# Kernel optimization log

Hardware: AMD Instinct MI355X
Metric: run time of the kernel (lower is better)

The kernel has to match this reference:

```python
import jax, jax.numpy as jnp
import numpy as np

B, T, C, S, H, K = 32, 128, 32, 256, 64, 3  # T == 2*H required by final Linear(hidden*2, 1)


def setup_inputs() -> dict:
    key = jax.random.key(0)
    k1, k2, k3, k4 = jax.random.split(key, 4)
    x = jax.random.normal(k1, (B, T, C, S), jnp.float32)
    # ConvLSTMCell: Conv1d(C+H -> 4H, kernel K, padding same), gate order i,f,o,g
    Wc = jax.random.normal(k2, (4 * H, C + H, K), jnp.float32) * 0.05
    bc = jnp.zeros((4 * H,), jnp.float32)
    # final Linear(hidden*2 = T, 1)
    Wl = jax.random.normal(k3, (1, T), jnp.float32) * 0.05
    bl = jnp.zeros((1,), jnp.float32)
    return {"x": x, "Wc": Wc, "bc": bc, "Wl": Wl, "bl": bl}


def _cell(x_t, h, c, Wc, bc):
    # x_t: (B, C, T); h, c: (B, H, T). Conv over the T axis, 'same' padding.
    z = jnp.concatenate([x_t, h], axis=1)  # (B, C+H, T)
    conv = jax.lax.conv_general_dilated(
        z, Wc, window_strides=(1,), padding='SAME',
        dimension_numbers=('NCH', 'OIH', 'NCH')) + bc[None, :, None]
    ci, cf, co, cg = jnp.split(conv, 4, axis=1)
    i = jax.nn.sigmoid(ci)
    f = jax.nn.sigmoid(cf)
    o = jax.nn.sigmoid(co)
    g = jnp.tanh(cg)
    c_next = f * c + i * g
    h_next = o * jnp.tanh(c_next)
    return h_next, c_next


def reference(x, Wc, bc, Wl, bl):
    # x: (B, T, C, S); sequential scan over spatial axis S with (h, c) recurrence.
    xs = jnp.transpose(x, (3, 0, 2, 1))  # (S, B, C, T)
    h0 = jnp.zeros((x.shape[0], H, x.shape[1]), x.dtype)

    def step(carry, xt):
        h, c = carry
        h2, c2 = _cell(xt, h, c, Wc, bc)
        return (h2, c2), h2

    _, hs = jax.lax.scan(step, (h0, h0), xs)  # hs: (S, B, H, T)
    lstm_out = jnp.transpose(hs, (1, 0, 2, 3))  # (B, S, H, T)
    out = jax.nn.sigmoid(jnp.einsum('bsht,ot->bso', lstm_out, Wl)[..., None].squeeze(-1)[..., None] * 0 + jnp.einsum('bsht,ot->bsho', lstm_out, Wl) + bl)
    return out  # (B, S, H, 1)
```

## Files before the change

### kernel.cpp

```cpp
#include <hip/hip_runtime.h>


#define Bb 32
#define Tt 128
#define Cc 32
#define Ss 256
#define Hh 64

typedef __bf16 bf16x8 __attribute__((ext_vector_type(8)));
typedef short  short8 __attribute__((ext_vector_type(8)));
typedef float  f32x4  __attribute__((ext_vector_type(4)));
typedef unsigned short u16;
typedef unsigned int   u32;

__device__ __forceinline__ u16 f2bf(float f) {
    u32 u = __float_as_uint(f);
    u = (u + 0x7FFFu + ((u >> 16) & 1u)) >> 16;
    return (u16)u;
}
__device__ __forceinline__ float fsig(float x) {
    float e = __expf(-x);
    return __builtin_amdgcn_rcpf(1.0f + e);
}
__device__ __forceinline__ float ftanh_(float x) {
    float e = __expf(2.0f * x);
    return 1.0f - 2.0f * __builtin_amdgcn_rcpf(e + 1.0f);
}

__global__ __launch_bounds__(256) void xpose_kernel(const float* __restrict__ x,
                                                    u16* __restrict__ xT) {
    __shared__ u16 tile[64][130];
    const int tc0 = blockIdx.x * 128;
    const int s0  = blockIdx.y * 64;
    const int b   = blockIdx.z;
    const int tid = threadIdx.x;
    const float* xb = x + (size_t)b * (Tt * Cc * Ss);
#pragma unroll
    for (int i = 0; i < 32; ++i) {
        const int tcr = (tid >> 6) + 4 * i;
        const int sr  = tid & 63;
        tile[sr][tcr] = f2bf(xb[(size_t)(tc0 + tcr) * Ss + s0 + sr]);
    }
    __syncthreads();
    u32* xTo = (u32*)(xT + (size_t)b * (Ss * Tt * Cc));
#pragma unroll
    for (int j = 0; j < 16; ++j) {
        const int sw = (tid >> 6) + 4 * j;
        const int tw = (tid & 63) * 2;
        xTo[(((size_t)(s0 + sw)) * (Tt * Cc) + tc0 + tw) >> 1] = *(const u32*)&tile[sw][tw];
    }
}

__global__ __launch_bounds__(512, 2) void convlstm_kernel(
    const float* __restrict__ Wc, const float* __restrict__ bc,
    const float* __restrict__ Wl, const float* __restrict__ bl,
    const u16* __restrict__ xT, float* __restrict__ out) {

    __shared__ u16  zbuf[2][130][104];
    __shared__ float red[8][16];
    __shared__ float bcl[256];

    const int b    = blockIdx.x;
    const int tid  = threadIdx.x;
    const int w    = tid >> 6;
    const int lane = tid & 63;
    const int l15  = lane & 15;
    const int q    = lane >> 4;
    const int ht   = w >> 1;
    const int th   = w & 1;

    {
        u32* z32 = (u32*)&zbuf[0][0][0];
        for (int i = tid; i < (2 * 130 * 104) / 2; i += 512) z32[i] = 0;
    }
    if (tid < 256) bcl[tid] = bc[tid];

    bf16x8 afr[4][3][3];
#pragma unroll
    for (int g = 0; g < 4; ++g) {
#pragma unroll
        for (int k = 0; k < 3; ++k) {
#pragma unroll
            for (int ks = 0; ks < 3; ++ks) {
                const int gc = 64 * g + 16 * ht + l15;
                short8 t;
#pragma unroll
                for (int j = 0; j < 8; ++j) {
                    const int c = 32 * ks + 8 * q + j;
                    t[j] = (short)f2bf(Wc[gc * 288 + c * 3 + k]);
                }
                afr[g][k][ks] = __builtin_bit_cast(bf16x8, t);
            }
        }
    }

    float wlv[4];
#pragma unroll
    for (int nj = 0; nj < 4; ++nj) wlv[nj] = Wl[64 * th + 16 * nj + l15];
    const float bl0 = bl[0];

    float cst[16];
#pragma unroll
    for (int i = 0; i < 16; ++i) cst[i] = 0.0f;

    const int xt = tid >> 2;
    const int xc = (tid & 3) * 8;
    const u16* xTb = xT + (size_t)b * (Ss * Tt * Cc);

    {
        uint4 xv0 = *(const uint4*)(xTb + 0 + xt * 32 + xc);
        __syncthreads();
        *(uint4*)&zbuf[0][1 + xt][xc] = xv0;
        __syncthreads();
    }

    float* outb = out + (size_t)b * (Ss * Hh);
    int p = 0;

    for (int s = 0; s < Ss; ++s) {
        uint4 xv;
        const bool havex = (s + 1) < Ss;
        if (havex) xv = *(const uint4*)(xTb + (size_t)(s + 1) * (Tt * Cc) + xt * 32 + xc);

        if (tid < 64 && s > 0) {
            float v = red[(tid >> 4) * 2][tid & 15] + red[(tid >> 4) * 2 + 1][tid & 15] + bl0;
            outb[(size_t)(s - 1) * Hh + tid] = fsig(v);
        }
        __syncthreads();

        const u16 (*zb)[104] = zbuf[p];
        u16 (*zn)[104] = zbuf[p ^ 1];

        float partial[4] = {0.f, 0.f, 0.f, 0.f};

#pragma unroll
        for (int half = 0; half < 2; ++half) {
            f32x4 acc[4][2];
#pragma unroll
            for (int g = 0; g < 4; ++g)
#pragma unroll
                for (int njl = 0; njl < 2; ++njl)
                    acc[g][njl] = (f32x4){0.f, 0.f, 0.f, 0.f};

#pragma unroll
            for (int njl = 0; njl < 2; ++njl) {
                const int nj = half * 2 + njl;
                const int tb = 64 * th + 16 * nj + l15;
#pragma unroll
                for (int k = 0; k < 3; ++k) {
#pragma unroll
                    for (int ks = 0; ks < 3; ++ks) {
                        bf16x8 bfr = *(const bf16x8*)&zb[tb + k][32 * ks + 8 * q];
                        acc[0][njl] = __builtin_amdgcn_mfma_f32_16x16x32_bf16(afr[0][k][ks], bfr, acc[0][njl], 0, 0, 0);
                        acc[1][njl] = __builtin_amdgcn_mfma_f32_16x16x32_bf16(afr[1][k][ks], bfr, acc[1][njl], 0, 0, 0);
                        acc[2][njl] = __builtin_amdgcn_mfma_f32_16x16x32_bf16(afr[2][k][ks], bfr, acc[2][njl], 0, 0, 0);
                        acc[3][njl] = __builtin_amdgcn_mfma_f32_16x16x32_bf16(afr[3][k][ks], bfr, acc[3][njl], 0, 0, 0);
                    }
                }
            }

#pragma unroll
            for (int njl = 0; njl < 2; ++njl) {
                const int nj = half * 2 + njl;
                u16 hp[4];
#pragma unroll
                for (int r = 0; r < 4; ++r) {
                    const int hl = 4 * q + r;
                    const float ci  = acc[0][njl][r] + bcl[0   + 16 * ht + hl];
                    const float cf  = acc[1][njl][r] + bcl[64  + 16 * ht + hl];
                    const float cop = acc[2][njl][r] + bcl[128 + 16 * ht + hl];
                    const float cg  = acc[3][njl][r] + bcl[192 + 16 * ht + hl];
                    const float ig = fsig(ci);
                    const float fg = fsig(cf);
                    const float og = fsig(cop);
                    const float gg = ftanh_(cg);
                    const float cv = fg * cst[nj * 4 + r] + ig * gg;
                    cst[nj * 4 + r] = cv;
                    const float hv = og * ftanh_(cv);
                    partial[r] += hv * wlv[nj];
                    hp[r] = f2bf(hv);
                }
                uint2 hw;
                hw.x = (u32)hp[0] | ((u32)hp[1] << 16);
                hw.y = (u32)hp[2] | ((u32)hp[3] << 16);
                *(uint2*)&zn[1 + 64 * th + 16 * nj + l15][32 + 16 * ht + 4 * q] = hw;
            }
        }

        if (havex) *(uint4*)&zn[1 + xt][xc] = xv;

#pragma unroll
        for (int r = 0; r < 4; ++r) {
#pragma unroll
            for (int off = 1; off <= 8; off <<= 1)
                partial[r] += __shfl_xor(partial[r], off, 64);
        }
        if (l15 == 0) {
#pragma unroll
            for (int r = 0; r < 4; ++r) red[w][4 * q + r] = partial[r];
        }
        __syncthreads();
        p ^= 1;
    }

    if (tid < 64) {
        float v = red[(tid >> 4) * 2][tid & 15] + red[(tid >> 4) * 2 + 1][tid & 15] + bl0;
        outb[(size_t)(Ss - 1) * Hh + tid] = fsig(v);
    }
}

extern "C" void kernel_launch(void* const* d_in, const int* in_sizes, int n_in,
                              void* d_out, int out_size, void* d_ws, size_t ws_size,
                              hipStream_t stream) {
    const float* x  = (const float*)d_in[0];
    const float* Wc = (const float*)d_in[1];
    const float* bc = (const float*)d_in[2];
    const float* Wl = (const float*)d_in[3];
    const float* bl = (const float*)d_in[4];
    float* out = (float*)d_out;
    u16*   xT  = (u16*)d_ws;

    dim3 tgrid(Tt * Cc / 128, Ss / 64, Bb);
    xpose_kernel<<<tgrid, 256, 0, stream>>>(x, xT);
    convlstm_kernel<<<Bb, 512, 0, stream>>>(Wc, bc, Wl, bl, xT, out);
}
```

Before: 1.273 ms.

## Precompute input-to-gate convolution in parallel kernel, shrink recurrent GEMM to hidden part

Splits the gate convolution into an input part and a recurrent part. The input part does not depend on the recurrence, so a new fully parallel kernel computes it for all timesteps and stores it in bf16 in workspace. The sequential kernel then only multiplies the hidden state (K=64 instead of 96) and loads the precomputed gate contributions one step ahead, software-pipelining the MFMA work against the gate math. The cost is about 512MB of extra global traffic, an extra bf16 rounding of the gate pre-activations, and a dependence on the workspace being large enough, with a fallback to the old kernel otherwise.

```diff
diff --git a/kernel.cpp b/kernel.cpp
--- a/kernel.cpp
+++ b/kernel.cpp
@@ -18,6 +18,8 @@
     u = (u + 0x7FFFu + ((u >> 16) & 1u)) >> 16;
     return (u16)u;
 }
+__device__ __forceinline__ float bfl(u32 d) { return __uint_as_float(d << 16); }
+__device__ __forceinline__ float bfh(u32 d) { return __uint_as_float(d & 0xffff0000u); }
 __device__ __forceinline__ float fsig(float x) {
     float e = __expf(-x);
     return __builtin_amdgcn_rcpf(1.0f + e);
@@ -48,6 +50,224 @@
         const int sw = (tid >> 6) + 4 * j;
         const int tw = (tid & 63) * 2;
         xTo[(((size_t)(s0 + sw)) * (Tt * Cc) + tc0 + tw) >> 1] = *(const u32*)&tile[sw][tw];
+    }
+}
+
+__global__ __launch_bounds__(256) void gatex_kernel(
+    const float* __restrict__ Wc, const float* __restrict__ bc,
+    const u16* __restrict__ xT, u16* __restrict__ gateX) {
+
+    __shared__ u16 zx[130][40];
+    const int s   = blockIdx.x;
+    const int b   = blockIdx.y;
+    const int tid = threadIdx.x;
+    const int g   = tid >> 6;
+    const int lane = tid & 63;
+    const int l15 = lane & 15;
+    const int q   = lane >> 4;
+
+    if (tid < 40) {
+        u32* zp = (u32*)&zx[(tid < 20) ? 0 : 129][0];
+        zp[(tid < 20) ? tid : tid - 20] = 0;
+    }
+    const u16* xp = xT + ((size_t)b * Ss + s) * (Tt * Cc);
+#pragma unroll
+    for (int i = 0; i < 4; ++i) {
+        const int idx = tid + 256 * i;
+        const int e = idx * 4;
+        *(uint2*)&zx[1 + (e >> 5)][e & 31] = *(const uint2*)(xp + e);
+    }
+
+    bf16x8 afr[4][3];
+#pragma unroll
+    for (int mt = 0; mt < 4; ++mt)
+#pragma unroll
+        for (int k = 0; k < 3; ++k) {
+            const int gc = 64 * g + 16 * mt + l15;
+            short8 t;
+#pragma unroll
+            for (int j = 0; j < 8; ++j) t[j] = (short)f2bf(Wc[gc * 288 + (8 * q + j) * 3 + k]);
+            afr[mt][k] = __builtin_bit_cast(bf16x8, t);
+        }
+    f32x4 bcv[4];
+#pragma unroll
+    for (int mt = 0; mt < 4; ++mt) bcv[mt] = *(const f32x4*)&bc[64 * g + 16 * mt + 4 * q];
+
+    __syncthreads();
+
+    u16* gxo = gateX + ((size_t)b * Ss + s) * (64 * 128 * 4);
+#pragma unroll
+    for (int nt = 0; nt < 8; ++nt) {
+        f32x4 acc[4];
+#pragma unroll
+        for (int mt = 0; mt < 4; ++mt) acc[mt] = bcv[mt];
+#pragma unroll
+        for (int k = 0; k < 3; ++k) {
+            bf16x8 bfr = *(const bf16x8*)&zx[16 * nt + l15 + k][8 * q];
+            acc[0] = __builtin_amdgcn_mfma_f32_16x16x32_bf16(afr[0][k], bfr, acc[0], 0, 0, 0);
+            acc[1] = __builtin_amdgcn_mfma_f32_16x16x32_bf16(afr[1][k], bfr, acc[1], 0, 0, 0);
+            acc[2] = __builtin_amdgcn_mfma_f32_16x16x32_bf16(afr[2][k], bfr, acc[2], 0, 0, 0);
+            acc[3] = __builtin_amdgcn_mfma_f32_16x16x32_bf16(afr[3][k], bfr, acc[3], 0, 0, 0);
+        }
+#pragma unroll
+        for (int mt = 0; mt < 4; ++mt) {
+            uint2 hw;
+            hw.x = (u32)f2bf(acc[mt][0]) | ((u32)f2bf(acc[mt][1]) << 16);
+            hw.y = (u32)f2bf(acc[mt][2]) | ((u32)f2bf(acc[mt][3]) << 16);
+            const int gcq = 16 * g + 4 * mt + q;
+            *(uint2*)(gxo + ((size_t)gcq * 128 + 16 * nt + l15) * 4) = hw;
+        }
+    }
+}
+
+__global__ __launch_bounds__(512, 2) void convlstm_gx_kernel(
+    const float* __restrict__ Wc, const float* __restrict__ Wl,
+    const float* __restrict__ bl, const u16* __restrict__ gateX,
+    float* __restrict__ out) {
+
+    __shared__ u16  zbuf[2][130][72];
+    __shared__ float red[2][8][16];
+
+    const int b    = blockIdx.x;
+    const int tid  = threadIdx.x;
+    const int w    = tid >> 6;
+    const int lane = tid & 63;
+    const int l15  = lane & 15;
+    const int q    = lane >> 4;
+    const int ht   = w >> 1;
+    const int th   = w & 1;
+
+    {
+        u32* z32 = (u32*)&zbuf[0][0][0];
+        for (int i = tid; i < (2 * 130 * 72) / 2; i += 512) z32[i] = 0;
+    }
+
+    bf16x8 afr[4][3][2];
+#pragma unroll
+    for (int g = 0; g < 4; ++g)
+#pragma unroll
+        for (int k = 0; k < 3; ++k)
+#pragma unroll
+            for (int ks = 0; ks < 2; ++ks) {
+                const int gc = 64 * g + 16 * ht + l15;
+                short8 t;
+#pragma unroll
+                for (int j = 0; j < 8; ++j)
+                    t[j] = (short)f2bf(Wc[gc * 288 + (32 + 32 * ks + 8 * q + j) * 3 + k]);
+                afr[g][k][ks] = __builtin_bit_cast(bf16x8, t);
+            }
+
+    float wlv[4];
+#pragma unroll
+    for (int nj = 0; nj < 4; ++nj) wlv[nj] = Wl[64 * th + 16 * nj + l15];
+    const float bl0 = bl[0];
+
+    float cst[16];
+#pragma unroll
+    for (int i = 0; i < 16; ++i) cst[i] = 0.0f;
+
+    const u16* gxb = gateX + (size_t)b * Ss * (64 * 128 * 4);
+    int off[16];
+#pragma unroll
+    for (int nj = 0; nj < 4; ++nj)
+#pragma unroll
+        for (int g = 0; g < 4; ++g)
+            off[nj * 4 + g] = (((16 * g + 4 * ht + q) * 128) + 64 * th + 16 * nj + l15) * 4;
+
+    uint2 gx[16];
+#pragma unroll
+    for (int i = 0; i < 16; ++i) gx[i] = *(const uint2*)(gxb + off[i]);
+
+    __syncthreads();
+
+    float* outb = out + (size_t)b * (Ss * Hh);
+
+    for (int s = 0; s < Ss; ++s) {
+        if (tid < 64 && s > 0) {
+            const int ps = (s - 1) & 1;
+            float v = red[ps][(tid >> 4) * 2][tid & 15] + red[ps][(tid >> 4) * 2 + 1][tid & 15] + bl0;
+            outb[(size_t)(s - 1) * Hh + tid] = fsig(v);
+        }
+
+        const u16 (*zb)[72] = zbuf[(s & 1) ^ 1];
+        u16 (*zn)[72] = zbuf[s & 1];
+
+        float partial[4] = {0.f, 0.f, 0.f, 0.f};
+        f32x4 acc[2][4];
+
+#pragma unroll
+        for (int c = 0; c < 5; ++c) {
+            if (c < 4) {
+                {
+                    const uint2 v0 = gx[c * 4 + 0], v1 = gx[c * 4 + 1];
+                    const uint2 v2 = gx[c * 4 + 2], v3 = gx[c * 4 + 3];
+                    acc[c & 1][0] = (f32x4){bfl(v0.x), bfh(v0.x), bfl(v0.y), bfh(v0.y)};
+                    acc[c & 1][1] = (f32x4){bfl(v1.x), bfh(v1.x), bfl(v1.y), bfh(v1.y)};
+                    acc[c & 1][2] = (f32x4){bfl(v2.x), bfh(v2.x), bfl(v2.y), bfh(v2.y)};
+                    acc[c & 1][3] = (f32x4){bfl(v3.x), bfh(v3.x), bfl(v3.y), bfh(v3.y)};
+                }
+                if (c == 3 && s + 1 < Ss) {
+                    const u16* gs = gxb + (size_t)(s + 1) * (64 * 128 * 4);
+#pragma unroll
+                    for (int i = 0; i < 16; ++i) gx[i] = *(const uint2*)(gs + off[i]);
+                }
+                {
+                    const int tb = 64 * th + 16 * c + l15;
+#pragma unroll
+                    for (int k = 0; k < 3; ++k)
+#pragma unroll
+                        for (int ks = 0; ks < 2; ++ks) {
+                            bf16x8 bfr = *(const bf16x8*)&zb[tb + k][32 * ks + 8 * q];
+                            acc[c & 1][0] = __builtin_amdgcn_mfma_f32_16x16x32_bf16(afr[0][k][ks], bfr, acc[c & 1][0], 0, 0, 0);
+                            acc[c & 1][1] = __builtin_amdgcn_mfma_f32_16x16x32_bf16(afr[1][k][ks], bfr, acc[c & 1][1], 0, 0, 0);
+                            acc[c & 1][2] = __builtin_amdgcn_mfma_f32_16x16x32_bf16(afr[2][k][ks], bfr, acc[c & 1][2], 0, 0, 0);
+                            acc[c & 1][3] = __builtin_amdgcn_mfma_f32_16x16x32_bf16(afr[3][k][ks], bfr, acc[c & 1][3], 0, 0, 0);
+                        }
+                }
+            }
+            if (c > 0) {
+                const int nj = c - 1;
+                u16 hp[4];
+#pragma unroll
+                for (int r = 0; r < 4; ++r) {
+                    const float ci  = acc[nj & 1][0][r];
+                    const float cf  = acc[nj & 1][1][r];
+                    const float cop = acc[nj & 1][2][r];
+                    const float cg  = acc[nj & 1][3][r];
+                    const float ig = fsig(ci);
+                    const float fg = fsig(cf);
+                    const float og = fsig(cop);
+                    const float gg = ftanh_(cg);
+                    const float cv = fg * cst[nj * 4 + r] + ig * gg;
+                    cst[nj * 4 + r] = cv;
+                    const float hv = og * ftanh_(cv);
+                    partial[r] += hv * wlv[nj];
+                    hp[r] = f2bf(hv);
+                }
+                uint2 hw;
+                hw.x = (u32)hp[0] | ((u32)hp[1] << 16);
+                hw.y = (u32)hp[2] | ((u32)hp[3] << 16);
+                *(uint2*)&zn[1 + 64 * th + 16 * nj + l15][16 * ht + 4 * q] = hw;
+            }
+        }
+
+#pragma unroll
+        for (int r = 0; r < 4; ++r) {
+#pragma unroll
+            for (int offl = 1; offl <= 8; offl <<= 1)
+                partial[r] += __shfl_xor(partial[r], offl, 64);
+        }
+        if (l15 == 0) {
+#pragma unroll
+            for (int r = 0; r < 4; ++r) red[s & 1][w][4 * q + r] = partial[r];
+        }
+        __syncthreads();
+    }
+
+    if (tid < 64) {
+        const int ps = (Ss - 1) & 1;
+        float v = red[ps][(tid >> 4) * 2][tid & 15] + red[ps][(tid >> 4) * 2 + 1][tid & 15] + bl0;
+        outb[(size_t)(Ss - 1) * Hh + tid] = fsig(v);
     }
 }
 
@@ -192,8 +412,8 @@
 #pragma unroll
         for (int r = 0; r < 4; ++r) {
 #pragma unroll
-            for (int off = 1; off <= 8; off <<= 1)
-                partial[r] += __shfl_xor(partial[r], off, 64);
+            for (int offl = 1; offl <= 8; offl <<= 1)
+                partial[r] += __shfl_xor(partial[r], offl, 64);
         }
         if (l15 == 0) {
 #pragma unroll
@@ -218,9 +438,19 @@
     const float* Wl = (const float*)d_in[3];
     const float* bl = (const float*)d_in[4];
     float* out = (float*)d_out;
-    u16*   xT  = (u16*)d_ws;
+
+    u16* xT = (u16*)d_ws;
+    const size_t XT_BYTES = (size_t)Bb * Ss * Tt * Cc * 2;
+    const size_t GX_BYTES = (size_t)Bb * Ss * 4 * Hh * Tt * 2;
 
     dim3 tgrid(Tt * Cc / 128, Ss / 64, Bb);
     xpose_kernel<<<tgrid, 256, 0, stream>>>(x, xT);
-    convlstm_kernel<<<Bb, 512, 0, stream>>>(Wc, bc, Wl, bl, xT, out);
-}
+
+    if (ws_size >= XT_BYTES + GX_BYTES) {
+        u16* gateX = (u16*)((char*)d_ws + XT_BYTES);
+        gatex_kernel<<<dim3(Ss, Bb), 256, 0, stream>>>(Wc, bc, xT, gateX);
+        convlstm_gx_kernel<<<Bb, 512, 0, stream>>>(Wc, Wl, bl, gateX, out);
+    } else {
+        convlstm_kernel<<<Bb, 512, 0, stream>>>(Wc, bc, Wl, bl, xT, out);
+    }
+}
```

Result: no change. 1.273 ms (+0.0%).

## Software-pipeline MFMA and gate math, drop one barrier per step, fold bias

Applied to the files above, without the earlier changes.

Restructures the per-step loop so the MFMA chunk for the next 16-column tile is issued before the gate math of the previous tile, letting matrix and vector work overlap. It removes one __syncthreads per recurrence step by double-buffering the reduction array. It also preloads the bias into the accumulator instead of reading it from LDS, changes the LDS row stride to 136 (likely to reduce bank conflicts), and packs bf16 with a hardware convert instruction. The costs are higher register pressure from two live accumulator sets and reliance on inline asm.

```diff
diff --git a/kernel.cpp b/kernel.cpp
--- a/kernel.cpp
+++ b/kernel.cpp
@@ -6,6 +6,7 @@
 #define Cc 32
 #define Ss 256
 #define Hh 64
+#define ZST 136
 
 typedef __bf16 bf16x8 __attribute__((ext_vector_type(8)));
 typedef short  short8 __attribute__((ext_vector_type(8)));
@@ -25,6 +26,11 @@
 __device__ __forceinline__ float ftanh_(float x) {
     float e = __expf(2.0f * x);
     return 1.0f - 2.0f * __builtin_amdgcn_rcpf(e + 1.0f);
+}
+__device__ __forceinline__ u32 cvtpk(float lo, float hi) {
+    u32 d;
+    asm("v_cvt_pk_bf16_f32 %0, %1, %2" : "=v"(d) : "v"(lo), "v"(hi));
+    return d;
 }
 
 __global__ __launch_bounds__(256) void xpose_kernel(const float* __restrict__ x,
@@ -51,14 +57,13 @@
     }
 }
 
-__global__ __launch_bounds__(512, 2) void convlstm_kernel(
+__global__ __launch_bounds__(512, 2) void convlstm3_kernel(
     const float* __restrict__ Wc, const float* __restrict__ bc,
     const float* __restrict__ Wl, const float* __restrict__ bl,
     const u16* __restrict__ xT, float* __restrict__ out) {
 
-    __shared__ u16  zbuf[2][130][104];
-    __shared__ float red[8][16];
-    __shared__ float bcl[256];
+    __shared__ u16  zbuf[2][130][ZST];
+    __shared__ float red[2][8][16];
 
     const int b    = blockIdx.x;
     const int tid  = threadIdx.x;
@@ -71,32 +76,38 @@
 
     {
         u32* z32 = (u32*)&zbuf[0][0][0];
-        for (int i = tid; i < (2 * 130 * 104) / 2; i += 512) z32[i] = 0;
-    }
-    if (tid < 256) bcl[tid] = bc[tid];
+        for (int i = tid; i < (2 * 130 * ZST) / 2; i += 512) z32[i] = 0;
+    }
 
     bf16x8 afr[4][3][3];
 #pragma unroll
-    for (int g = 0; g < 4; ++g) {
-#pragma unroll
-        for (int k = 0; k < 3; ++k) {
+    for (int g = 0; g < 4; ++g)
+#pragma unroll
+        for (int k = 0; k < 3; ++k)
 #pragma unroll
             for (int ks = 0; ks < 3; ++ks) {
                 const int gc = 64 * g + 16 * ht + l15;
                 short8 t;
 #pragma unroll
-                for (int j = 0; j < 8; ++j) {
-                    const int c = 32 * ks + 8 * q + j;
-                    t[j] = (short)f2bf(Wc[gc * 288 + c * 3 + k]);
-                }
-                afr[g][k][ks] = __builtin_bit_cast(bf16x8, t);
+                for (int j = 0; j < 8; ++j)
+                    t[j] = (short)f2bf(Wc[gc * 288 + (32 * ks + 8 * q + j) * 3 + k]);
+                f32x4 kv = __builtin_bit_cast(f32x4, t);
+                asm volatile("" : "+v"(kv));
+                afr[g][k][ks] = __builtin_bit_cast(bf16x8, kv);
             }
-        }
-    }
-
+
+    f32x4 bcv[4];
+#pragma unroll
+    for (int g = 0; g < 4; ++g) {
+        bcv[g] = *(const f32x4*)&bc[64 * g + 16 * ht + 4 * q];
+        asm volatile("" : "+v"(bcv[g]));
+    }
     float wlv[4];
 #pragma unroll
-    for (int nj = 0; nj < 4; ++nj) wlv[nj] = Wl[64 * th + 16 * nj + l15];
+    for (int nj = 0; nj < 4; ++nj) {
+        wlv[nj] = Wl[64 * th + 16 * nj + l15];
+        asm volatile("" : "+v"(wlv[nj]));
+    }
     const float bl0 = bl[0];
 
     float cst[16];
@@ -108,14 +119,13 @@
     const u16* xTb = xT + (size_t)b * (Ss * Tt * Cc);
 
     {
-        uint4 xv0 = *(const uint4*)(xTb + 0 + xt * 32 + xc);
+        uint4 xv0 = *(const uint4*)(xTb + xt * 32 + xc);
         __syncthreads();
-        *(uint4*)&zbuf[0][1 + xt][xc] = xv0;
+        *(uint4*)&zbuf[1][1 + xt][xc] = xv0;
         __syncthreads();
     }
 
     float* outb = out + (size_t)b * (Ss * Hh);
-    int p = 0;
 
     for (int s = 0; s < Ss; ++s) {
         uint4 xv;
@@ -123,66 +133,51 @@
         if (havex) xv = *(const uint4*)(xTb + (size_t)(s + 1) * (Tt * Cc) + xt * 32 + xc);
 
         if (tid < 64 && s > 0) {
-            float v = red[(tid >> 4) * 2][tid & 15] + red[(tid >> 4) * 2 + 1][tid & 15] + bl0;
+            const int ps = (s - 1) & 1;
+            float v = red[ps][(tid >> 4) * 2][tid & 15] + red[ps][(tid >> 4) * 2 + 1][tid & 15] + bl0;
             outb[(size_t)(s - 1) * Hh + tid] = fsig(v);
         }
-        __syncthreads();
-
-        const u16 (*zb)[104] = zbuf[p];
-        u16 (*zn)[104] = zbuf[p ^ 1];
+
+        const u16 (*zb)[ZST] = zbuf[(s & 1) ^ 1];
+        u16 (*zn)[ZST] = zbuf[s & 1];
 
         float partial[4] = {0.f, 0.f, 0.f, 0.f};
-
-#pragma unroll
-        for (int half = 0; half < 2; ++half) {
-            f32x4 acc[4][2];
-#pragma unroll
-            for (int g = 0; g < 4; ++g)
-#pragma unroll
-                for (int njl = 0; njl < 2; ++njl)
-                    acc[g][njl] = (f32x4){0.f, 0.f, 0.f, 0.f};
-
-#pragma unroll
-            for (int njl = 0; njl < 2; ++njl) {
-                const int nj = half * 2 + njl;
-                const int tb = 64 * th + 16 * nj + l15;
-#pragma unroll
-                for (int k = 0; k < 3; ++k) {
+        f32x4 acc[2][4];
+
+#pragma unroll
+        for (int c = 0; c < 5; ++c) {
+            if (c < 4) {
+#pragma unroll
+                for (int g = 0; g < 4; ++g) acc[c & 1][g] = bcv[g];
+                const int tb = 64 * th + 16 * c + l15;
+#pragma unroll
+                for (int k = 0; k < 3; ++k)
 #pragma unroll
                     for (int ks = 0; ks < 3; ++ks) {
                         bf16x8 bfr = *(const bf16x8*)&zb[tb + k][32 * ks + 8 * q];
-                        acc[0][njl] = __builtin_amdgcn_mfma_f32_16x16x32_bf16(afr[0][k][ks], bfr, acc[0][njl], 0, 0, 0);
-                        acc[1][njl] = __builtin_amdgcn_mfma_f32_16x16x32_bf16(afr[1][k][ks], bfr, acc[1][njl], 0, 0, 0);
-                        acc[2][njl] = __builtin_amdgcn_mfma_f32_16x16x32_bf16(afr[2][k][ks], bfr, acc[2][njl], 0, 0, 0);
-                        acc[3][njl] = __builtin_amdgcn_mfma_f32_16x16x32_bf16(afr[3][k][ks], bfr, acc[3][njl], 0, 0, 0);
+                        acc[c & 1][0] = __builtin_amdgcn_mfma_f32_16x16x32_bf16(afr[0][k][ks], bfr, acc[c & 1][0], 0, 0, 0);
+                        acc[c & 1][1] = __builtin_amdgcn_mfma_f32_16x16x32_bf16(afr[1][k][ks], bfr, acc[c & 1][1], 0, 0, 0);
+                        acc[c & 1][2] = __builtin_amdgcn_mfma_f32_16x16x32_bf16(afr[2][k][ks], bfr, acc[c & 1][2], 0, 0, 0);
+                        acc[c & 1][3] = __builtin_amdgcn_mfma_f32_16x16x32_bf16(afr[3][k][ks], bfr, acc[c & 1][3], 0, 0, 0);
                     }
-                }
             }
-
-#pragma unroll
-            for (int njl = 0; njl < 2; ++njl) {
-                const int nj = half * 2 + njl;
-                u16 hp[4];
+            if (c > 0) {
+                const int nj = c - 1;
+                float hv[4];
 #pragma unroll
                 for (int r = 0; r < 4; ++r) {
-                    const int hl = 4 * q + r;
-                    const float ci  = acc[0][njl][r] + bcl[0   + 16 * ht + hl];
-                    const float cf  = acc[1][njl][r] + bcl[64  + 16 * ht + hl];
-                    const float cop = acc[2][njl][r] + bcl[128 + 16 * ht + hl];
-                    const float cg  = acc[3][njl][r] + bcl[192 + 16 * ht + hl];
-                    const float ig = fsig(ci);
-                    const float fg = fsig(cf);
-                    const float og = fsig(cop);
-                    const float gg = ftanh_(cg);
+                    const float ig = fsig(acc[nj & 1][0][r]);
+                    const float fg = fsig(acc[nj & 1][1][r]);
+                    const float og = fsig(acc[nj & 1][2][r]);
+                    const float gg = ftanh_(acc[nj & 1][3][r]);
                     const float cv = fg * cst[nj * 4 + r] + ig * gg;
                     cst[nj * 4 + r] = cv;
-                    const float hv = og * ftanh_(cv);
-                    partial[r] += hv * wlv[nj];
-                    hp[r] = f2bf(hv);
+                    hv[r] = og * ftanh_(cv);
+                    partial[r] += hv[r] * wlv[nj];
                 }
                 uint2 hw;
-                hw.x = (u32)hp[0] | ((u32)hp[1] << 16);
-                hw.y = (u32)hp[2] | ((u32)hp[3] << 16);
+                hw.x = cvtpk(hv[0], hv[1]);
+                hw.y = cvtpk(hv[2], hv[3]);
                 *(uint2*)&zn[1 + 64 * th + 16 * nj + l15][32 + 16 * ht + 4 * q] = hw;
             }
         }
@@ -192,19 +187,19 @@
 #pragma unroll
         for (int r = 0; r < 4; ++r) {
 #pragma unroll
-            for (int off = 1; off <= 8; off <<= 1)
-                partial[r] += __shfl_xor(partial[r], off, 64);
+            for (int offl = 1; offl <= 8; offl <<= 1)
+                partial[r] += __shfl_xor(partial[r], offl, 64);
         }
         if (l15 == 0) {
 #pragma unroll
-            for (int r = 0; r < 4; ++r) red[w][4 * q + r] = partial[r];
+            for (int r = 0; r < 4; ++r) red[s & 1][w][4 * q + r] = partial[r];
         }
         __syncthreads();
-        p ^= 1;
     }
 
     if (tid < 64) {
-        float v = red[(tid >> 4) * 2][tid & 15] + red[(tid >> 4) * 2 + 1][tid & 15] + bl0;
+        const int ps = (Ss - 1) & 1;
+        float v = red[ps][(tid >> 4) * 2][tid & 15] + red[ps][(tid >> 4) * 2 + 1][tid & 15] + bl0;
         outb[(size_t)(Ss - 1) * Hh + tid] = fsig(v);
     }
 }
@@ -222,5 +217,5 @@
 
     dim3 tgrid(Tt * Cc / 128, Ss / 64, Bb);
     xpose_kernel<<<tgrid, 256, 0, stream>>>(x, xT);
-    convlstm_kernel<<<Bb, 512, 0, stream>>>(Wc, bc, Wl, bl, xT, out);
-}
+    convlstm3_kernel<<<Bb, 512, 0, stream>>>(Wc, bc, Wl, bl, xT, out);
+}
```

Measured after the change: 1.449 ms. 1.14x slower.

## Stream pre-swizzled bf16 conv weights from global instead of holding them in registers

Applied to the files above, without the earlier changes.

A new prep kernel converts Wc into the MFMA A-fragment layout in bf16 and stores it in workspace. The main recurrent kernel then reloads these fragments from global/L2 every step with a double-buffered prefetch, instead of keeping 36 bf16x8 fragments per lane in registers. The conv bias is folded into the accumulator init, which removes the per-element LDS bias reads. The aim is to free a large amount of register pressure, at the cost of per-step weight loads whose latency may land on the serial critical path. The old kernel is kept as a fallback when the workspace is too small.

```diff
diff --git a/kernel.cpp b/kernel.cpp
--- a/kernel.cpp
+++ b/kernel.cpp
@@ -6,6 +6,7 @@
 #define Cc 32
 #define Ss 256
 #define Hh 64
+#define ZST 104
 
 typedef __bf16 bf16x8 __attribute__((ext_vector_type(8)));
 typedef short  short8 __attribute__((ext_vector_type(8)));
@@ -51,14 +52,36 @@
     }
 }
 
-__global__ __launch_bounds__(512, 2) void convlstm_kernel(
-    const float* __restrict__ Wc, const float* __restrict__ bc,
-    const float* __restrict__ Wl, const float* __restrict__ bl,
-    const u16* __restrict__ xT, float* __restrict__ out) {
-
-    __shared__ u16  zbuf[2][130][104];
+__global__ __launch_bounds__(256) void wprep_kernel(const float* __restrict__ Wc,
+                                                    u16* __restrict__ wpre) {
+    const int ht  = blockIdx.x;
+    const int tid = threadIdx.x;
+#pragma unroll
+    for (int it = 0; it < 9; ++it) {
+        const int idx  = it * 256 + tid;
+        const int f    = idx >> 6;
+        const int lane = idx & 63;
+        const int g  = f / 9;
+        const int k  = (f % 9) / 3;
+        const int ks = f % 3;
+        const int l15 = lane & 15;
+        const int q   = lane >> 4;
+        const int gc  = 64 * g + 16 * ht + l15;
+        u16 tmp[8];
+#pragma unroll
+        for (int j = 0; j < 8; ++j)
+            tmp[j] = f2bf(Wc[gc * 288 + (32 * ks + 8 * q + j) * 3 + k]);
+        *(uint4*)(wpre + ((size_t)(ht * 36 + f) * 64 + lane) * 8) = *(const uint4*)tmp;
+    }
+}
+
+__global__ __launch_bounds__(512) void convlstm5_kernel(
+    const float* __restrict__ bc, const float* __restrict__ Wl,
+    const float* __restrict__ bl, const u16* __restrict__ xT,
+    const u16* __restrict__ wpre, float* __restrict__ out) {
+
+    __shared__ u16  zbuf[2][130][ZST];
     __shared__ float red[8][16];
-    __shared__ float bcl[256];
 
     const int b    = blockIdx.x;
     const int tid  = threadIdx.x;
@@ -71,29 +94,14 @@
 
     {
         u32* z32 = (u32*)&zbuf[0][0][0];
-        for (int i = tid; i < (2 * 130 * 104) / 2; i += 512) z32[i] = 0;
-    }
-    if (tid < 256) bcl[tid] = bc[tid];
-
-    bf16x8 afr[4][3][3];
-#pragma unroll
-    for (int g = 0; g < 4; ++g) {
-#pragma unroll
-        for (int k = 0; k < 3; ++k) {
-#pragma unroll
-            for (int ks = 0; ks < 3; ++ks) {
-                const int gc = 64 * g + 16 * ht + l15;
-                short8 t;
-#pragma unroll
-                for (int j = 0; j < 8; ++j) {
-                    const int c = 32 * ks + 8 * q + j;
-                    t[j] = (short)f2bf(Wc[gc * 288 + c * 3 + k]);
-                }
-                afr[g][k][ks] = __builtin_bit_cast(bf16x8, t);
-            }
-        }
-    }
-
+        for (int i = tid; i < (2 * 130 * ZST) / 2; i += 512) z32[i] = 0;
+    }
+
+    const u16* wlp = wpre + (size_t)ht * 18432 + lane * 8;
+
+    f32x4 bcv[4];
+#pragma unroll
+    for (int g = 0; g < 4; ++g) bcv[g] = *(const f32x4*)&bc[64 * g + 16 * ht + 4 * q];
     float wlv[4];
 #pragma unroll
     for (int nj = 0; nj < 4; ++nj) wlv[nj] = Wl[64 * th + 16 * nj + l15];
@@ -108,7 +116,7 @@
     const u16* xTb = xT + (size_t)b * (Ss * Tt * Cc);
 
     {
-        uint4 xv0 = *(const uint4*)(xTb + 0 + xt * 32 + xc);
+        uint4 xv0 = *(const uint4*)(xTb + xt * 32 + xc);
         __syncthreads();
         *(uint4*)&zbuf[0][1 + xt][xc] = xv0;
         __syncthreads();
@@ -128,8 +136,8 @@
         }
         __syncthreads();
 
-        const u16 (*zb)[104] = zbuf[p];
-        u16 (*zn)[104] = zbuf[p ^ 1];
+        const u16 (*zb)[ZST] = zbuf[p];
+        u16 (*zn)[ZST] = zbuf[p ^ 1];
 
         float partial[4] = {0.f, 0.f, 0.f, 0.f};
 
@@ -137,25 +145,35 @@
         for (int half = 0; half < 2; ++half) {
             f32x4 acc[4][2];
 #pragma unroll
+            for (int g = 0; g < 4; ++g) {
+                acc[g][0] = bcv[g];
+                acc[g][1] = bcv[g];
+            }
+
+            bf16x8 wf[2][4];
+#pragma unroll
             for (int g = 0; g < 4; ++g)
-#pragma unroll
-                for (int njl = 0; njl < 2; ++njl)
-                    acc[g][njl] = (f32x4){0.f, 0.f, 0.f, 0.f};
-
-#pragma unroll
-            for (int njl = 0; njl < 2; ++njl) {
-                const int nj = half * 2 + njl;
-                const int tb = 64 * th + 16 * nj + l15;
-#pragma unroll
-                for (int k = 0; k < 3; ++k) {
-#pragma unroll
-                    for (int ks = 0; ks < 3; ++ks) {
-                        bf16x8 bfr = *(const bf16x8*)&zb[tb + k][32 * ks + 8 * q];
-                        acc[0][njl] = __builtin_amdgcn_mfma_f32_16x16x32_bf16(afr[0][k][ks], bfr, acc[0][njl], 0, 0, 0);
-                        acc[1][njl] = __builtin_amdgcn_mfma_f32_16x16x32_bf16(afr[1][k][ks], bfr, acc[1][njl], 0, 0, 0);
-                        acc[2][njl] = __builtin_amdgcn_mfma_f32_16x16x32_bf16(afr[2][k][ks], bfr, acc[2][njl], 0, 0, 0);
-                        acc[3][njl] = __builtin_amdgcn_mfma_f32_16x16x32_bf16(afr[3][k][ks], bfr, acc[3][njl], 0, 0, 0);
-                    }
+                wf[0][g] = *(const bf16x8*)(wlp + (size_t)(g * 9) * 512);
+
+#pragma unroll
+            for (int kk = 0; kk < 9; ++kk) {
+                const int k  = kk / 3;
+                const int ks = kk % 3;
+                const int cur = kk & 1;
+                if (kk < 8) {
+#pragma unroll
+                    for (int g = 0; g < 4; ++g)
+                        wf[cur ^ 1][g] = *(const bf16x8*)(wlp + (size_t)(g * 9 + kk + 1) * 512);
+                }
+#pragma unroll
+                for (int njl = 0; njl < 2; ++njl) {
+                    const int nj = half * 2 + njl;
+                    const int tb = 64 * th + 16 * nj + l15;
+                    bf16x8 bfr = *(const bf16x8*)&zb[tb + k][32 * ks + 8 * q];
+                    acc[0][njl] = __builtin_amdgcn_mfma_f32_16x16x32_bf16(wf[cur][0], bfr, acc[0][njl], 0, 0, 0);
+                    acc[1][njl] = __builtin_amdgcn_mfma_f32_16x16x32_bf16(wf[cur][1], bfr, acc[1][njl], 0, 0, 0);
+                    acc[2][njl] = __builtin_amdgcn_mfma_f32_16x16x32_bf16(wf[cur][2], bfr, acc[2][njl], 0, 0, 0);
+                    acc[3][njl] = __builtin_amdgcn_mfma_f32_16x16x32_bf16(wf[cur][3], bfr, acc[3][njl], 0, 0, 0);
                 }
             }
 
@@ -165,15 +183,10 @@
                 u16 hp[4];
 #pragma unroll
                 for (int r = 0; r < 4; ++r) {
-                    const int hl = 4 * q + r;
-                    const float ci  = acc[0][njl][r] + bcl[0   + 16 * ht + hl];
-                    const float cf  = acc[1][njl][r] + bcl[64  + 16 * ht + hl];
-                    const float cop = acc[2][njl][r] + bcl[128 + 16 * ht + hl];
-                    const float cg  = acc[3][njl][r] + bcl[192 + 16 * ht + hl];
-                    const float ig = fsig(ci);
-                    const float fg = fsig(cf);
-                    const float og = fsig(cop);
-                    const float gg = ftanh_(cg);
+                    const float ig = fsig(acc[0][njl][r]);
+                    const float fg = fsig(acc[1][njl][r]);
+                    const float og = fsig(acc[2][njl][r]);
+                    const float gg = ftanh_(acc[3][njl][r]);
                     const float cv = fg * cst[nj * 4 + r] + ig * gg;
                     cst[nj * 4 + r] = cv;
                     const float hv = og * ftanh_(cv);
@@ -192,8 +205,156 @@
 #pragma unroll
         for (int r = 0; r < 4; ++r) {
 #pragma unroll
-            for (int off = 1; off <= 8; off <<= 1)
-                partial[r] += __shfl_xor(partial[r], off, 64);
+            for (int offl = 1; offl <= 8; offl <<= 1)
+                partial[r] += __shfl_xor(partial[r], offl, 64);
+        }
+        if (l15 == 0) {
+#pragma unroll
+            for (int r = 0; r < 4; ++r) red[w][4 * q + r] = partial[r];
+        }
+        __syncthreads();
+        p ^= 1;
+    }
+
+    if (tid < 64) {
+        float v = red[(tid >> 4) * 2][tid & 15] + red[(tid >> 4) * 2 + 1][tid & 15] + bl0;
+        outb[(size_t)(Ss - 1) * Hh + tid] = fsig(v);
+    }
+}
+
+__global__ __launch_bounds__(512, 2) void convlstm_kernel(
+    const float* __restrict__ Wc, const float* __restrict__ bc,
+    const float* __restrict__ Wl, const float* __restrict__ bl,
+    const u16* __restrict__ xT, float* __restrict__ out) {
+
+    __shared__ u16  zbuf[2][130][ZST];
+    __shared__ float red[8][16];
+    __shared__ float bcl[256];
+
+    const int b    = blockIdx.x;
+    const int tid  = threadIdx.x;
+    const int w    = tid >> 6;
+    const int lane = tid & 63;
+    const int l15  = lane & 15;
+    const int q    = lane >> 4;
+    const int ht   = w >> 1;
+    const int th   = w & 1;
+
+    {
+        u32* z32 = (u32*)&zbuf[0][0][0];
+        for (int i = tid; i < (2 * 130 * ZST) / 2; i += 512) z32[i] = 0;
+    }
+    if (tid < 256) bcl[tid] = bc[tid];
+
+    bf16x8 afr[4][3][3];
+#pragma unroll
+    for (int g = 0; g < 4; ++g)
+#pragma unroll
+        for (int k = 0; k < 3; ++k)
+#pragma unroll
+            for (int ks = 0; ks < 3; ++ks) {
+                const int gc = 64 * g + 16 * ht + l15;
+                short8 t;
+#pragma unroll
+                for (int j = 0; j < 8; ++j)
+                    t[j] = (short)f2bf(Wc[gc * 288 + (32 * ks + 8 * q + j) * 3 + k]);
+                afr[g][k][ks] = __builtin_bit_cast(bf16x8, t);
+            }
+
+    float wlv[4];
+#pragma unroll
+    for (int nj = 0; nj < 4; ++nj) wlv[nj] = Wl[64 * th + 16 * nj + l15];
+    const float bl0 = bl[0];
+
+    float cst[16];
+#pragma unroll
+    for (int i = 0; i < 16; ++i) cst[i] = 0.0f;
+
+    const int xt = tid >> 2;
+    const int xc = (tid & 3) * 8;
+    const u16* xTb = xT + (size_t)b * (Ss * Tt * Cc);
+
+    {
+        uint4 xv0 = *(const uint4*)(xTb + xt * 32 + xc);
+        __syncthreads();
+        *(uint4*)&zbuf[0][1 + xt][xc] = xv0;
+        __syncthreads();
+    }
+
+    float* outb = out + (size_t)b * (Ss * Hh);
+    int p = 0;
+
+    for (int s = 0; s < Ss; ++s) {
+        uint4 xv;
+        const bool havex = (s + 1) < Ss;
+        if (havex) xv = *(const uint4*)(xTb + (size_t)(s + 1) * (Tt * Cc) + xt * 32 + xc);
+
+        if (tid < 64 && s > 0) {
+            float v = red[(tid >> 4) * 2][tid & 15] + red[(tid >> 4) * 2 + 1][tid & 15] + bl0;
+            outb[(size_t)(s - 1) * Hh + tid] = fsig(v);
+        }
+        __syncthreads();
+
+        const u16 (*zb)[ZST] = zbuf[p];
+        u16 (*zn)[ZST] = zbuf[p ^ 1];
+
+        float partial[4] = {0.f, 0.f, 0.f, 0.f};
+
+#pragma unroll
+        for (int half = 0; half < 2; ++half) {
+            f32x4 acc[4][2];
+#pragma unroll
+            for (int g = 0; g < 4; ++g) {
+                acc[g][0] = (f32x4){0.f, 0.f, 0.f, 0.f};
+                acc[g][1] = (f32x4){0.f, 0.f, 0.f, 0.f};
+            }
+#pragma unroll
+            for (int njl = 0; njl < 2; ++njl) {
+                const int nj = half * 2 + njl;
+                const int tb = 64 * th + 16 * nj + l15;
+#pragma unroll
+                for (int k = 0; k < 3; ++k)
+#pragma unroll
+                    for (int ks = 0; ks < 3; ++ks) {
+                        bf16x8 bfr = *(const bf16x8*)&zb[tb + k][32 * ks + 8 * q];
+                        acc[0][njl] = __builtin_amdgcn_mfma_f32_16x16x32_bf16(afr[0][k][ks], bfr, acc[0][njl], 0, 0, 0);
+                        acc[1][njl] = __builtin_amdgcn_mfma_f32_16x16x32_bf16(afr[1][k][ks], bfr, acc[1][njl], 0, 0, 0);
+                        acc[2][njl] = __builtin_amdgcn_mfma_f32_16x16x32_bf16(afr[2][k][ks], bfr, acc[2][njl], 0, 0, 0);
+                        acc[3][njl] = __builtin_amdgcn_mfma_f32_16x16x32_bf16(afr[3][k][ks], bfr, acc[3][njl], 0, 0, 0);
+                    }
+            }
+
+#pragma unroll
+            for (int njl = 0; njl < 2; ++njl) {
+                const int nj = half * 2 + njl;
+                u16 hp[4];
+#pragma unroll
+                for (int r = 0; r < 4; ++r) {
+                    const int hl = 4 * q + r;
+                    const float ig = fsig(acc[0][njl][r] + bcl[0   + 16 * ht + hl]);
+                    const float fg = fsig(acc[1][njl][r] + bcl[64  + 16 * ht + hl]);
+                    const float og = fsig(acc[2][njl][r] + bcl[128 + 16 * ht + hl]);
+                    const float gg = ftanh_(acc[3][njl][r] + bcl[192 + 16 * ht + hl]);
+                    const float cv = fg * cst[nj * 4 + r] + ig * gg;
+                    cst[nj * 4 + r] = cv;
+                    const float hv = og * ftanh_(cv);
+                    partial[r] += hv * wlv[nj];
+                    hp[r] = f2bf(hv);
+                }
+                uint2 hw;
+                hw.x = (u32)hp[0] | ((u32)hp[1] << 16);
+                hw.y = (u32)hp[2] | ((u32)hp[3] << 16);
+                *(uint2*)&zn[1 + 64 * th + 16 * nj + l15][32 + 16 * ht + 4 * q] = hw;
+            }
+        }
+
+        if (havex) *(uint4*)&zn[1 + xt][xc] = xv;
+
+#pragma unroll
+        for (int r = 0; r < 4; ++r) {
+#pragma unroll
+            for (int offl = 1; offl <= 8; offl <<= 1)
+                partial[r] += __shfl_xor(partial[r], offl, 64);
         }
         if (l15 == 0) {
 #pragma unroll
@@ -218,9 +379,19 @@
     const float* Wl = (const float*)d_in[3];
     const float* bl = (const float*)d_in[4];
     float* out = (float*)d_out;
-    u16*   xT  = (u16*)d_ws;
+
+    u16* xT = (u16*)d_ws;
+    const size_t XT_BYTES = (size_t)Bb * Ss * Tt * Cc * 2;
+    const size_t WP_BYTES = (size_t)4 * 36 * 64 * 8 * 2;
 
     dim3 tgrid(Tt * Cc / 128, Ss / 64, Bb);
     xpose_kernel<<<tgrid, 256, 0, stream>>>(x, xT);
-    convlstm_kernel<<<Bb, 512, 0, stream>>>(Wc, bc, Wl, bl, xT, out);
-}
+
+    if (ws_size >= XT_BYTES + WP_BYTES) {
+        u16* wpre = (u16*)((char*)d_ws + XT_BYTES);
+        wprep_kernel<<<4, 256, 0, stream>>>(Wc, wpre);
+        convlstm5_kernel<<<Bb, 512, 0, stream>>>(bc, Wl, bl, xT, wpre, out);
+    } else {
+        convlstm_kernel<<<Bb, 512, 0, stream>>>(Wc, bc, Wl, bl, xT, out);
+    }
+}
```

Result: slower. 1.375 ms (+8.0%).
